# Kernel tuning notes

Hardware: AMD Instinct MI355X
Metric: run time of the kernel (lower is better)

Reference implementation:

```python
import jax, jax.numpy as jnp
import numpy as np

B, N, D, P = 64, 1024, 256, 256


def setup_inputs() -> dict:
    key = jax.random.key(0)
    kx, k1, k2, k4 = jax.random.split(key, 4)
    x = jax.random.normal(kx, (B, N, D), dtype=jnp.float32)
    # weights ~ random_uniform(-0.05, 0.05) in the original; scale here is irrelevant for math
    w1 = jax.random.uniform(k1, (D, P), dtype=jnp.float32, minval=-0.05, maxval=0.05)
    w2 = jax.random.uniform(k2, (D, P), dtype=jnp.float32, minval=-0.05, maxval=0.05)
    w4 = jax.random.uniform(k4, (P, 1), dtype=jnp.float32, minval=-0.05, maxval=0.05)
    return {"x": x, "w1": w1, "w2": w2, "w4": w4}


def reference(x, w1, w2, w4):
    # x: [B, N, D] (already stacked/transposed; query_n=key_n=values=x in the original)
    q = jax.nn.sigmoid(jnp.einsum('bnd,dp->bnp', x, w1))  # [B,N,P]
    k = jax.nn.sigmoid(jnp.einsum('bnd,dp->bnp', x, w2))  # [B,N,P]
    temper = jnp.sqrt(jnp.asarray(w1.shape[1], x.dtype))
    attn = jax.nn.softmax(jnp.einsum('bnp,bmp->bnm', q, k) / temper, axis=2)  # [B,N,N]
    # dropout(0.1) in the original is inference-identity here
    out = jnp.einsum('bnm,bmd->bnd', attn, x)             # [B,N,D]
    a = jax.nn.softmax(jnp.einsum('bnd,do->bno', out, w4), axis=1)  # [B,N,1]
    sentence = jnp.sum(x * a, axis=1)                     # [B,D]
    return sentence
```

## Files before the change

### kernel.cpp

```cpp
#include <hip/hip_runtime.h>
#include <hip/hip_bf16.h>
#include <cstdint>
#include <cstddef>

constexpr int BB = 64;
constexpr int NN = 1024;
constexpr int DD = 256;
constexpr int PP = 256;

typedef short short8 __attribute__((ext_vector_type(8)));
typedef float f32x4 __attribute__((ext_vector_type(4)));

constexpr float LOG2E = 1.4426950408889634f;

__device__ __forceinline__ unsigned short f2bf(float f) {
    union { __hip_bfloat16 h; unsigned short u; } v;
    v.h = __float2bfloat16(f);
    return v.u;
}

__device__ __forceinline__ float fsigmoid(float x) {
    return __builtin_amdgcn_rcpf(1.f + __builtin_amdgcn_exp2f(x * -LOG2E));
}

__device__ __forceinline__ void pin8(short8& v) {
    asm volatile("" : "+v"(v));
}

__device__ __forceinline__ void async_load16(void* lds, const void* g) {
    __builtin_amdgcn_global_load_lds(
        (const __attribute__((address_space(1))) unsigned int*)g,
        (__attribute__((address_space(3))) unsigned int*)lds, 16, 0, 0);
}

__device__ __forceinline__ void stage256(const unsigned short* base,
                                         unsigned short* lds, int wv, int lane) {
    char* dst0 = (char*)lds + wv * 16384;
    #pragma unroll
    for (int i = 0; i < 16; i++) {
        int row = wv * 32 + i * 2 + (lane >> 5);
        int blk = (lane & 31) ^ (row & 7);
        async_load16(dst0 + i * 1024, (const char*)base + row * 512 + blk * 16);
    }
}

__device__ __forceinline__ short8 lds_frag(const unsigned short* lds, int row, int kidx) {
    uint32_t byte = (uint32_t)(row * 512) + (uint32_t)(((kidx ^ (row & 7)) & 31) << 4);
    return *reinterpret_cast<const short8*>(reinterpret_cast<const char*>(lds) + byte);
}

__global__ void prep_wt(const float* __restrict__ w1, const float* __restrict__ w2,
                        unsigned short* __restrict__ wt) {
    int j = blockIdx.x;
    int d = threadIdx.x;
    const float* w = (j < PP) ? w1 : w2;
    int jj = j & (PP - 1);
    wt[j * DD + d] = f2bf(w[d * PP + jj]);
}

__global__ __launch_bounds__(512, 2) void qk_fused(const float* __restrict__ x,
                                                   const unsigned short* __restrict__ wt,
                                                   const float* __restrict__ w4,
                                                   unsigned short* __restrict__ qb,
                                                   unsigned short* __restrict__ kb,
                                                   float* __restrict__ xv) {
    __shared__ __align__(16) unsigned short wl[256 * 256];
    const int t = threadIdx.x, wv = t >> 6, lane = t & 63, l15 = lane & 15, l4 = lane >> 4;
    const int rowBase = blockIdx.x * 256 + wv * 32;

    stage256(wt, wl, wv, lane);

    short8 xf[2][8];
    float xvp[2] = {0.f, 0.f};
    #pragma unroll
    for (int kc = 0; kc < 8; kc++) {
        float4 w4a = *reinterpret_cast<const float4*>(w4 + kc * 32 + l4 * 8);
        float4 w4b = *reinterpret_cast<const float4*>(w4 + kc * 32 + l4 * 8 + 4);
        #pragma unroll
        for (int s = 0; s < 2; s++) {
            const float* xr = x + (size_t)(rowBase + s * 16 + l15) * DD + kc * 32 + l4 * 8;
            float4 a = *reinterpret_cast<const float4*>(xr);
            float4 b = *reinterpret_cast<const float4*>(xr + 4);
            xvp[s] += a.x * w4a.x + a.y * w4a.y + a.z * w4a.z + a.w * w4a.w
                    + b.x * w4b.x + b.y * w4b.y + b.z * w4b.z + b.w * w4b.w;
            short8 f;
            f[0] = (short)f2bf(a.x); f[1] = (short)f2bf(a.y);
            f[2] = (short)f2bf(a.z); f[3] = (short)f2bf(a.w);
            f[4] = (short)f2bf(b.x); f[5] = (short)f2bf(b.y);
            f[6] = (short)f2bf(b.z); f[7] = (short)f2bf(b.w);
            xf[s][kc] = f;
        }
    }
    #pragma unroll
    for (int s = 0; s < 2; s++)
        #pragma unroll
        for (int kc = 0; kc < 8; kc++) pin8(xf[s][kc]);
    #pragma unroll
    for (int s = 0; s < 2; s++) {
        xvp[s] += __shfl_xor(xvp[s], 16);
        xvp[s] += __shfl_xor(xvp[s], 32);
        if (l4 == 0) xv[rowBase + s * 16 + l15] = xvp[s];
    }

    __syncthreads();

    #pragma unroll 1
    for (int h = 0; h < 2; h++) {
        if (h == 1) {
            __syncthreads();
            stage256(wt + 256 * DD, wl, wv, lane);
            __syncthreads();
        }
        unsigned short* outp = h ? kb : qb;
        #pragma unroll 1
        for (int pt = 0; pt < 16; pt++) {
            f32x4 acc0 = {0.f, 0.f, 0.f, 0.f};
            f32x4 acc1 = {0.f, 0.f, 0.f, 0.f};
            __builtin_amdgcn_s_setprio(1);
            #pragma unroll
            for (int kc = 0; kc < 8; kc++) {
                short8 wf = lds_frag(wl, pt * 16 + l15, kc * 4 + l4);
                acc0 = __builtin_amdgcn_mfma_f32_16x16x32_bf16(wf, xf[0][kc], acc0, 0, 0, 0);
                acc1 = __builtin_amdgcn_mfma_f32_16x16x32_bf16(wf, xf[1][kc], acc1, 0, 0, 0);
            }
            __builtin_amdgcn_s_setprio(0);
            const int pc = pt * 16 + l4 * 4;
            ushort4 pk;
            pk.x = f2bf(fsigmoid(acc0[0]));
            pk.y = f2bf(fsigmoid(acc0[1]));
            pk.z = f2bf(fsigmoid(acc0[2]));
            pk.w = f2bf(fsigmoid(acc0[3]));
            *reinterpret_cast<ushort4*>(outp + (size_t)(rowBase + l15) * PP + pc) = pk;
            pk.x = f2bf(fsigmoid(acc1[0]));
            pk.y = f2bf(fsigmoid(acc1[1]));
            pk.z = f2bf(fsigmoid(acc1[2]));
            pk.w = f2bf(fsigmoid(acc1[3]));
            *reinterpret_cast<ushort4*>(outp + (size_t)(rowBase + 16 + l15) * PP + pc) = pk;
        }
    }
}

__global__ __launch_bounds__(512, 2) void attn_logit(const unsigned short* __restrict__ qb,
                                                     const unsigned short* __restrict__ kb,
                                                     const float* __restrict__ xv,
                                                     float* __restrict__ numo,
                                                     float* __restrict__ deno) {
    __shared__ __align__(16) unsigned short kq[256 * 256];
    __shared__ float xvs[256];
    const int t = threadIdx.x, wv = t >> 6, lane = t & 63, l15 = lane & 15, l4 = lane >> 4;
    const int wg = blockIdx.x;
    const int xcd = wg & 7, r_ = wg >> 3;
    const int quarter = r_ & 3;
    const int b = xcd + 8 * (r_ >> 2);
    const unsigned short* kbb = kb + ((size_t)b * NN + quarter * 256) * PP;

    stage256(kbb, kq, wv, lane);
    if (t < 256) xvs[t] = xv[b * NN + quarter * 256 + t];
    __syncthreads();

    #pragma unroll 1
    for (int p = 0; p < 2; p++) {
        short8 qf[4][8];
        const int q0 = b * NN + p * 512 + wv * 64;
        #pragma unroll
        for (int s = 0; s < 4; s++) {
            const unsigned short* qrow = qb + (size_t)(q0 + s * 16 + l15) * PP;
            #pragma unroll
            for (int kc = 0; kc < 8; kc++)
                qf[s][kc] = *reinterpret_cast<const short8*>(qrow + kc * 32 + l4 * 8);
        }
        #pragma unroll
        for (int s = 0; s < 4; s++)
            #pragma unroll
            for (int kc = 0; kc < 8; kc++) pin8(qf[s][kc]);

        float den[4][4], num[4][4];
        #pragma unroll
        for (int s = 0; s < 4; s++)
            #pragma unroll
            for (int r = 0; r < 4; r++) { den[s][r] = 0.f; num[s][r] = 0.f; }

        #pragma unroll 8
        for (int mc = 0; mc < 16; mc++) {
            f32x4 z = {0.f, 0.f, 0.f, 0.f};
            f32x4 a[4] = {z, z, z, z};
            __builtin_amdgcn_s_setprio(1);
            #pragma unroll
            for (int kc = 0; kc < 8; kc++) {
                short8 kf = lds_frag(kq, mc * 16 + l15, kc * 4 + l4);
                a[0] = __builtin_amdgcn_mfma_f32_16x16x32_bf16(qf[0][kc], kf, a[0], 0, 0, 0);
                a[1] = __builtin_amdgcn_mfma_f32_16x16x32_bf16(qf[1][kc], kf, a[1], 0, 0, 0);
                a[2] = __builtin_amdgcn_mfma_f32_16x16x32_bf16(qf[2][kc], kf, a[2], 0, 0, 0);
                a[3] = __builtin_amdgcn_mfma_f32_16x16x32_bf16(qf[3][kc], kf, a[3], 0, 0, 0);
            }
            __builtin_amdgcn_s_setprio(0);
            float xvv = xvs[mc * 16 + l15];
            #pragma unroll
            for (int s = 0; s < 4; s++)
                #pragma unroll
                for (int r = 0; r < 4; r++) {
                    float e = __builtin_amdgcn_exp2f(a[s][r] * (0.0625f * LOG2E));
                    den[s][r] += e;
                    num[s][r] += e * xvv;
                }
        }
        #pragma unroll
        for (int s = 0; s < 4; s++)
            #pragma unroll
            for (int r = 0; r < 4; r++) {
                #pragma unroll
                for (int off = 1; off < 16; off <<= 1) {
                    den[s][r] += __shfl_xor(den[s][r], off);
                    num[s][r] += __shfl_xor(num[s][r], off);
                }
            }
        if (l15 == 0) {
            #pragma unroll
            for (int s = 0; s < 4; s++)
                #pragma unroll
                for (int r = 0; r < 4; r++) {
                    int n = p * 512 + wv * 64 + s * 16 + l4 * 4 + r;
                    size_t o = (size_t)quarter * BB * NN + (size_t)b * NN + n;
                    numo[o] = num[s][r];
                    deno[o] = den[s][r];
                }
        }
    }
}

__global__ __launch_bounds__(256) void sent_partial(const float* __restrict__ x,
                                                    const float* __restrict__ numo,
                                                    const float* __restrict__ deno,
                                                    float* __restrict__ part) {
    __shared__ float al[64];
    __shared__ float redA[4];
    __shared__ float redB[4];
    const int b = blockIdx.x, ch = blockIdx.y;
    const int t = threadIdx.x;
    float l[4];
    #pragma unroll
    for (int i = 0; i < 4; i++) {
        int n = b * NN + t + i * 256;
        float ns = 0.f, ds = 0.f;
        #pragma unroll
        for (int q = 0; q < 4; q++) {
            ns += numo[(size_t)q * BB * NN + n];
            ds += deno[(size_t)q * BB * NN + n];
        }
        l[i] = ns / ds;
    }
    float mx = fmaxf(fmaxf(l[0], l[1]), fmaxf(l[2], l[3]));
    #pragma unroll
    for (int off = 1; off < 64; off <<= 1) mx = fmaxf(mx, __shfl_xor(mx, off));
    if ((t & 63) == 0) redA[t >> 6] = mx;
    __syncthreads();
    mx = fmaxf(fmaxf(redA[0], redA[1]), fmaxf(redA[2], redA[3]));
    float e[4], es = 0.f;
    #pragma unroll
    for (int i = 0; i < 4; i++) { e[i] = __expf(l[i] - mx); es += e[i]; }
    #pragma unroll
    for (int off = 1; off < 64; off <<= 1) es += __shfl_xor(es, off);
    if ((t & 63) == 0) redB[t >> 6] = es;
    __syncthreads();
    float inv = 1.f / (redB[0] + redB[1] + redB[2] + redB[3]);
    int ei = ch >> 2;
    float sel = (ei == 0) ? e[0] : (ei == 1) ? e[1] : (ei == 2) ? e[2] : e[3];
    if ((t >> 6) == (ch & 3)) al[t & 63] = sel * inv;
    __syncthreads();
    float acc = 0.f;
    const float* xb = x + ((size_t)b * NN + ch * 64) * DD + t;
    #pragma unroll 8
    for (int n = 0; n < 64; n++)
        acc += al[n] * xb[(size_t)n * DD];
    part[(b * 16 + ch) * DD + t] = acc;
}

__global__ void sent_final(const float* __restrict__ part, float* __restrict__ out) {
    int b = blockIdx.x, t = threadIdx.x;
    float s = 0.f;
    #pragma unroll
    for (int c = 0; c < 16; c++) s += part[(b * 16 + c) * DD + t];
    out[b * DD + t] = s;
}

extern "C" void kernel_launch(void* const* d_in, const int* in_sizes, int n_in,
                              void* d_out, int out_size, void* d_ws, size_t ws_size,
                              hipStream_t stream) {
    (void)in_sizes; (void)n_in; (void)out_size; (void)ws_size;
    const float* x  = (const float*)d_in[0];
    const float* w1 = (const float*)d_in[1];
    const float* w2 = (const float*)d_in[2];
    const float* w4 = (const float*)d_in[3];
    float* out = (float*)d_out;

    char* ws = (char*)d_ws;
    const size_t MB = 1024 * 1024;
    unsigned short* qb   = (unsigned short*)(ws);
    unsigned short* kb   = (unsigned short*)(ws + 32 * MB);
    unsigned short* wt   = (unsigned short*)(ws + 64 * MB);
    float*          xv   = (float*)(ws + 64 * MB + 256 * 1024);
    float*          num  = (float*)(ws + 64 * MB + 512 * 1024);
    float*          den  = (float*)(ws + 64 * MB + 1536 * 1024);
    float*          part = (float*)(ws);

    prep_wt<<<dim3(2 * PP), dim3(DD), 0, stream>>>(w1, w2, wt);
    qk_fused<<<dim3(BB * NN / 256), dim3(512), 0, stream>>>(x, wt, w4, qb, kb, xv);
    attn_logit<<<dim3(4 * BB), dim3(512), 0, stream>>>(qb, kb, xv, num, den);
    sent_partial<<<dim3(BB, 16), dim3(256), 0, stream>>>(x, num, den, part);
    sent_final<<<dim3(BB), dim3(DD), 0, stream>>>(part, out);
}
```

Before: 94.35 us.

## Compute K projection inside attn_logit directly into LDS instead of via global

Moves the K = sigmoid(x·W2) projection out of qk_fused and into attn_logit. Each block now loads its 256 rows of x, converts them to bf16, and multiplies them against W2, which is staged 32 columns at a time. The result is written straight into the swizzled LDS tile that used to be filled from kb. This removes the 32 MB bf16 K write and read-back through global memory and halves the projection work in qk_fused. The cost is extra x loads and MFMA work, plus eight barrier-separated W2 staging rounds inside the attention kernel, which may reduce its occupancy or overlap.

```diff
diff --git a/kernel.cpp b/kernel.cpp
--- a/kernel.cpp
+++ b/kernel.cpp
@@ -39,6 +39,17 @@
     #pragma unroll
     for (int i = 0; i < 16; i++) {
         int row = wv * 32 + i * 2 + (lane >> 5);
+        int blk = (lane & 31) ^ (row & 7);
+        async_load16(dst0 + i * 1024, (const char*)base + row * 512 + blk * 16);
+    }
+}
+
+__device__ __forceinline__ void stage32_w8(const unsigned short* base,
+                                           unsigned short* lds, int wv, int lane) {
+    char* dst0 = (char*)lds + wv * 2048;
+    #pragma unroll
+    for (int i = 0; i < 2; i++) {
+        int row = wv * 4 + i * 2 + (lane >> 5);
         int blk = (lane & 31) ^ (row & 7);
         async_load16(dst0 + i * 1024, (const char*)base + row * 512 + blk * 16);
     }
@@ -62,7 +73,6 @@
                                                    const unsigned short* __restrict__ wt,
                                                    const float* __restrict__ w4,
                                                    unsigned short* __restrict__ qb,
-                                                   unsigned short* __restrict__ kb,
                                                    float* __restrict__ xv) {
     __shared__ __align__(16) unsigned short wl[256 * 256];
     const int t = threadIdx.x, wv = t >> 6, lane = t & 63, l15 = lane & 15, l4 = lane >> 4;
@@ -105,58 +115,111 @@
     __syncthreads();
 
     #pragma unroll 1
-    for (int h = 0; h < 2; h++) {
-        if (h == 1) {
-            __syncthreads();
-            stage256(wt + 256 * DD, wl, wv, lane);
-            __syncthreads();
-        }
-        unsigned short* outp = h ? kb : qb;
-        #pragma unroll 1
-        for (int pt = 0; pt < 16; pt++) {
-            f32x4 acc0 = {0.f, 0.f, 0.f, 0.f};
-            f32x4 acc1 = {0.f, 0.f, 0.f, 0.f};
-            __builtin_amdgcn_s_setprio(1);
-            #pragma unroll
-            for (int kc = 0; kc < 8; kc++) {
-                short8 wf = lds_frag(wl, pt * 16 + l15, kc * 4 + l4);
-                acc0 = __builtin_amdgcn_mfma_f32_16x16x32_bf16(wf, xf[0][kc], acc0, 0, 0, 0);
-                acc1 = __builtin_amdgcn_mfma_f32_16x16x32_bf16(wf, xf[1][kc], acc1, 0, 0, 0);
-            }
-            __builtin_amdgcn_s_setprio(0);
-            const int pc = pt * 16 + l4 * 4;
-            ushort4 pk;
-            pk.x = f2bf(fsigmoid(acc0[0]));
-            pk.y = f2bf(fsigmoid(acc0[1]));
-            pk.z = f2bf(fsigmoid(acc0[2]));
-            pk.w = f2bf(fsigmoid(acc0[3]));
-            *reinterpret_cast<ushort4*>(outp + (size_t)(rowBase + l15) * PP + pc) = pk;
-            pk.x = f2bf(fsigmoid(acc1[0]));
-            pk.y = f2bf(fsigmoid(acc1[1]));
-            pk.z = f2bf(fsigmoid(acc1[2]));
-            pk.w = f2bf(fsigmoid(acc1[3]));
-            *reinterpret_cast<ushort4*>(outp + (size_t)(rowBase + 16 + l15) * PP + pc) = pk;
-        }
-    }
-}
-
-__global__ __launch_bounds__(512, 2) void attn_logit(const unsigned short* __restrict__ qb,
-                                                     const unsigned short* __restrict__ kb,
+    for (int pt = 0; pt < 16; pt++) {
+        f32x4 acc0 = {0.f, 0.f, 0.f, 0.f};
+        f32x4 acc1 = {0.f, 0.f, 0.f, 0.f};
+        __builtin_amdgcn_s_setprio(1);
+        #pragma unroll
+        for (int kc = 0; kc < 8; kc++) {
+            short8 wf = lds_frag(wl, pt * 16 + l15, kc * 4 + l4);
+            acc0 = __builtin_amdgcn_mfma_f32_16x16x32_bf16(wf, xf[0][kc], acc0, 0, 0, 0);
+            acc1 = __builtin_amdgcn_mfma_f32_16x16x32_bf16(wf, xf[1][kc], acc1, 0, 0, 0);
+        }
+        __builtin_amdgcn_s_setprio(0);
+        const int pc = pt * 16 + l4 * 4;
+        ushort4 pk;
+        pk.x = f2bf(fsigmoid(acc0[0]));
+        pk.y = f2bf(fsigmoid(acc0[1]));
+        pk.z = f2bf(fsigmoid(acc0[2]));
+        pk.w = f2bf(fsigmoid(acc0[3]));
+        *reinterpret_cast<ushort4*>(qb + (size_t)(rowBase + l15) * PP + pc) = pk;
+        pk.x = f2bf(fsigmoid(acc1[0]));
+        pk.y = f2bf(fsigmoid(acc1[1]));
+        pk.z = f2bf(fsigmoid(acc1[2]));
+        pk.w = f2bf(fsigmoid(acc1[3]));
+        *reinterpret_cast<ushort4*>(qb + (size_t)(rowBase + 16 + l15) * PP + pc) = pk;
+    }
+}
+
+__global__ __launch_bounds__(512, 2) void attn_logit(const float* __restrict__ x,
+                                                     const unsigned short* __restrict__ wt,
+                                                     const unsigned short* __restrict__ qb,
                                                      const float* __restrict__ xv,
                                                      float* __restrict__ numo,
                                                      float* __restrict__ deno) {
     __shared__ __align__(16) unsigned short kq[256 * 256];
+    __shared__ __align__(16) unsigned short wld[32 * 256];
     __shared__ float xvs[256];
     const int t = threadIdx.x, wv = t >> 6, lane = t & 63, l15 = lane & 15, l4 = lane >> 4;
     const int wg = blockIdx.x;
     const int xcd = wg & 7, r_ = wg >> 3;
     const int quarter = r_ & 3;
     const int b = xcd + 8 * (r_ >> 2);
-    const unsigned short* kbb = kb + ((size_t)b * NN + quarter * 256) * PP;
-
-    stage256(kbb, kq, wv, lane);
+    const unsigned short* wt2 = wt + 256 * DD;
+
+    stage32_w8(wt2, wld, wv, lane);
+
+    short8 xf[2][8];
+    const float* xq = x + (size_t)(b * NN + quarter * 256 + wv * 32) * DD;
+    #pragma unroll
+    for (int kc = 0; kc < 8; kc++) {
+        #pragma unroll
+        for (int s = 0; s < 2; s++) {
+            const float* xr = xq + (size_t)(s * 16 + l15) * DD + kc * 32 + l4 * 8;
+            float4 a = *reinterpret_cast<const float4*>(xr);
+            float4 bq = *reinterpret_cast<const float4*>(xr + 4);
+            short8 f;
+            f[0] = (short)f2bf(a.x);  f[1] = (short)f2bf(a.y);
+            f[2] = (short)f2bf(a.z);  f[3] = (short)f2bf(a.w);
+            f[4] = (short)f2bf(bq.x); f[5] = (short)f2bf(bq.y);
+            f[6] = (short)f2bf(bq.z); f[7] = (short)f2bf(bq.w);
+            xf[s][kc] = f;
+        }
+    }
+    #pragma unroll
+    for (int s = 0; s < 2; s++)
+        #pragma unroll
+        for (int kc = 0; kc < 8; kc++) pin8(xf[s][kc]);
     if (t < 256) xvs[t] = xv[b * NN + quarter * 256 + t];
-    __syncthreads();
+
+    __syncthreads();
+
+    #pragma unroll 1
+    for (int c = 0; c < 8; c++) {
+        __builtin_amdgcn_s_setprio(1);
+        #pragma unroll
+        for (int pt = 0; pt < 2; pt++) {
+            f32x4 acc0 = {0.f, 0.f, 0.f, 0.f};
+            f32x4 acc1 = {0.f, 0.f, 0.f, 0.f};
+            #pragma unroll
+            for (int kc = 0; kc < 8; kc++) {
+                short8 wf = lds_frag(wld, pt * 16 + l15, kc * 4 + l4);
+                acc0 = __builtin_amdgcn_mfma_f32_16x16x32_bf16(wf, xf[0][kc], acc0, 0, 0, 0);
+                acc1 = __builtin_amdgcn_mfma_f32_16x16x32_bf16(wf, xf[1][kc], acc1, 0, 0, 0);
+            }
+            const int p0 = c * 32 + pt * 16 + l4 * 4;
+            #pragma unroll
+            for (int s = 0; s < 2; s++) {
+                const f32x4& a = s ? acc1 : acc0;
+                ushort4 pk;
+                pk.x = f2bf(fsigmoid(a[0]));
+                pk.y = f2bf(fsigmoid(a[1]));
+                pk.z = f2bf(fsigmoid(a[2]));
+                pk.w = f2bf(fsigmoid(a[3]));
+                int m = wv * 32 + s * 16 + l15;
+                uint32_t byte = (uint32_t)(m * 512)
+                              + (uint32_t)((((p0 >> 3) ^ (m & 7)) & 31) << 4)
+                              + (uint32_t)((p0 & 7) * 2);
+                *reinterpret_cast<ushort4*>(reinterpret_cast<char*>(kq) + byte) = pk;
+            }
+        }
+        __builtin_amdgcn_s_setprio(0);
+        __syncthreads();
+        if (c < 7) {
+            stage32_w8(wt2 + (size_t)(c + 1) * 32 * DD, wld, wv, lane);
+            __syncthreads();
+        }
+    }
 
     #pragma unroll 1
     for (int p = 0; p < 2; p++) {
@@ -296,7 +359,6 @@
     char* ws = (char*)d_ws;
     const size_t MB = 1024 * 1024;
     unsigned short* qb   = (unsigned short*)(ws);
-    unsigned short* kb   = (unsigned short*)(ws + 32 * MB);
     unsigned short* wt   = (unsigned short*)(ws + 64 * MB);
     float*          xv   = (float*)(ws + 64 * MB + 256 * 1024);
     float*          num  = (float*)(ws + 64 * MB + 512 * 1024);
@@ -304,8 +366,8 @@
     float*          part = (float*)(ws);
 
     prep_wt<<<dim3(2 * PP), dim3(DD), 0, stream>>>(w1, w2, wt);
-    qk_fused<<<dim3(BB * NN / 256), dim3(512), 0, stream>>>(x, wt, w4, qb, kb, xv);
-    attn_logit<<<dim3(4 * BB), dim3(512), 0, stream>>>(qb, kb, xv, num, den);
+    qk_fused<<<dim3(BB * NN / 256), dim3(512), 0, stream>>>(x, wt, w4, qb, xv);
+    attn_logit<<<dim3(4 * BB), dim3(512), 0, stream>>>(x, wt, qb, xv, num, den);
     sent_partial<<<dim3(BB, 16), dim3(256), 0, stream>>>(x, num, den, part);
     sent_final<<<dim3(BB), dim3(DD), 0, stream>>>(part, out);
 }
```

Result: slower. 100.3 us (+6.3%).

## Split attention logit work across twice as many 1024-thread blocks

Applied to the files above, without the earlier changes.

Restructures attn_logit so each block handles half the queries for a key quarter, with 16 waves each owning 32 queries, instead of 8 waves looping over two 64-query passes. The aim is more resident waves per CU to hide latency, and lower per-wave register pressure. In exchange, each K tile is staged into LDS twice as often, and each LDS fragment now feeds only two MFMAs instead of four, which raises LDS read traffic.

```diff
diff --git a/kernel.cpp b/kernel.cpp
--- a/kernel.cpp
+++ b/kernel.cpp
@@ -33,12 +33,23 @@
         (__attribute__((address_space(3))) unsigned int*)lds, 16, 0, 0);
 }
 
-__device__ __forceinline__ void stage256(const unsigned short* base,
-                                         unsigned short* lds, int wv, int lane) {
+__device__ __forceinline__ void stage256_w8(const unsigned short* base,
+                                            unsigned short* lds, int wv, int lane) {
     char* dst0 = (char*)lds + wv * 16384;
     #pragma unroll
     for (int i = 0; i < 16; i++) {
         int row = wv * 32 + i * 2 + (lane >> 5);
+        int blk = (lane & 31) ^ (row & 7);
+        async_load16(dst0 + i * 1024, (const char*)base + row * 512 + blk * 16);
+    }
+}
+
+__device__ __forceinline__ void stage256_w16(const unsigned short* base,
+                                             unsigned short* lds, int wv, int lane) {
+    char* dst0 = (char*)lds + wv * 8192;
+    #pragma unroll
+    for (int i = 0; i < 8; i++) {
+        int row = wv * 16 + i * 2 + (lane >> 5);
         int blk = (lane & 31) ^ (row & 7);
         async_load16(dst0 + i * 1024, (const char*)base + row * 512 + blk * 16);
     }
@@ -68,7 +79,7 @@
     const int t = threadIdx.x, wv = t >> 6, lane = t & 63, l15 = lane & 15, l4 = lane >> 4;
     const int rowBase = blockIdx.x * 256 + wv * 32;
 
-    stage256(wt, wl, wv, lane);
+    stage256_w8(wt, wl, wv, lane);
 
     short8 xf[2][8];
     float xvp[2] = {0.f, 0.f};
@@ -108,7 +119,7 @@
     for (int h = 0; h < 2; h++) {
         if (h == 1) {
             __syncthreads();
-            stage256(wt + 256 * DD, wl, wv, lane);
+            stage256_w8(wt + 256 * DD, wl, wv, lane);
             __syncthreads();
         }
         unsigned short* outp = h ? kb : qb;
@@ -140,91 +151,86 @@
     }
 }
 
-__global__ __launch_bounds__(512, 2) void attn_logit(const unsigned short* __restrict__ qb,
-                                                     const unsigned short* __restrict__ kb,
-                                                     const float* __restrict__ xv,
-                                                     float* __restrict__ numo,
-                                                     float* __restrict__ deno) {
+__global__ __launch_bounds__(1024, 4) void attn_logit(const unsigned short* __restrict__ qb,
+                                                      const unsigned short* __restrict__ kb,
+                                                      const float* __restrict__ xv,
+                                                      float* __restrict__ numo,
+                                                      float* __restrict__ deno) {
     __shared__ __align__(16) unsigned short kq[256 * 256];
     __shared__ float xvs[256];
     const int t = threadIdx.x, wv = t >> 6, lane = t & 63, l15 = lane & 15, l4 = lane >> 4;
     const int wg = blockIdx.x;
     const int xcd = wg & 7, r_ = wg >> 3;
-    const int quarter = r_ & 3;
-    const int b = xcd + 8 * (r_ >> 2);
+    const int qhalf = r_ & 1;
+    const int quarter = (r_ >> 1) & 3;
+    const int b = (r_ >> 3) * 8 + xcd;
     const unsigned short* kbb = kb + ((size_t)b * NN + quarter * 256) * PP;
 
-    stage256(kbb, kq, wv, lane);
+    stage256_w16(kbb, kq, wv, lane);
     if (t < 256) xvs[t] = xv[b * NN + quarter * 256 + t];
     __syncthreads();
 
-    #pragma unroll 1
-    for (int p = 0; p < 2; p++) {
-        short8 qf[4][8];
-        const int q0 = b * NN + p * 512 + wv * 64;
-        #pragma unroll
-        for (int s = 0; s < 4; s++) {
-            const unsigned short* qrow = qb + (size_t)(q0 + s * 16 + l15) * PP;
+    short8 qf[2][8];
+    const int q0 = b * NN + qhalf * 512 + wv * 32;
+    #pragma unroll
+    for (int s = 0; s < 2; s++) {
+        const unsigned short* qrow = qb + (size_t)(q0 + s * 16 + l15) * PP;
+        #pragma unroll
+        for (int kc = 0; kc < 8; kc++)
+            qf[s][kc] = *reinterpret_cast<const short8*>(qrow + kc * 32 + l4 * 8);
+    }
+    #pragma unroll
+    for (int s = 0; s < 2; s++)
+        #pragma unroll
+        for (int kc = 0; kc < 8; kc++) pin8(qf[s][kc]);
+
+    float den[2][4], num[2][4];
+    #pragma unroll
+    for (int s = 0; s < 2; s++)
+        #pragma unroll
+        for (int r = 0; r < 4; r++) { den[s][r] = 0.f; num[s][r] = 0.f; }
+
+    #pragma unroll 8
+    for (int mc = 0; mc < 16; mc++) {
+        f32x4 a0 = {0.f, 0.f, 0.f, 0.f};
+        f32x4 a1 = {0.f, 0.f, 0.f, 0.f};
+        __builtin_amdgcn_s_setprio(1);
+        #pragma unroll
+        for (int kc = 0; kc < 8; kc++) {
+            short8 kf = lds_frag(kq, mc * 16 + l15, kc * 4 + l4);
+            a0 = __builtin_amdgcn_mfma_f32_16x16x32_bf16(qf[0][kc], kf, a0, 0, 0, 0);
+            a1 = __builtin_amdgcn_mfma_f32_16x16x32_bf16(qf[1][kc], kf, a1, 0, 0, 0);
+        }
+        __builtin_amdgcn_s_setprio(0);
+        float xvv = xvs[mc * 16 + l15];
+        #pragma unroll
+        for (int r = 0; r < 4; r++) {
+            float e0 = __builtin_amdgcn_exp2f(a0[r] * (0.0625f * LOG2E));
+            den[0][r] += e0; num[0][r] += e0 * xvv;
+            float e1 = __builtin_amdgcn_exp2f(a1[r] * (0.0625f * LOG2E));
+            den[1][r] += e1; num[1][r] += e1 * xvv;
+        }
+    }
+    #pragma unroll
+    for (int s = 0; s < 2; s++)
+        #pragma unroll
+        for (int r = 0; r < 4; r++) {
             #pragma unroll
-            for (int kc = 0; kc < 8; kc++)
-                qf[s][kc] = *reinterpret_cast<const short8*>(qrow + kc * 32 + l4 * 8);
-        }
-        #pragma unroll
-        for (int s = 0; s < 4; s++)
-            #pragma unroll
-            for (int kc = 0; kc < 8; kc++) pin8(qf[s][kc]);
-
-        float den[4][4], num[4][4];
-        #pragma unroll
-        for (int s = 0; s < 4; s++)
-            #pragma unroll
-            for (int r = 0; r < 4; r++) { den[s][r] = 0.f; num[s][r] = 0.f; }
-
-        #pragma unroll 8
-        for (int mc = 0; mc < 16; mc++) {
-            f32x4 z = {0.f, 0.f, 0.f, 0.f};
-            f32x4 a[4] = {z, z, z, z};
-            __builtin_amdgcn_s_setprio(1);
-            #pragma unroll
-            for (int kc = 0; kc < 8; kc++) {
-                short8 kf = lds_frag(kq, mc * 16 + l15, kc * 4 + l4);
-                a[0] = __builtin_amdgcn_mfma_f32_16x16x32_bf16(qf[0][kc], kf, a[0], 0, 0, 0);
-                a[1] = __builtin_amdgcn_mfma_f32_16x16x32_bf16(qf[1][kc], kf, a[1], 0, 0, 0);
-                a[2] = __builtin_amdgcn_mfma_f32_16x16x32_bf16(qf[2][kc], kf, a[2], 0, 0, 0);
-                a[3] = __builtin_amdgcn_mfma_f32_16x16x32_bf16(qf[3][kc], kf, a[3], 0, 0, 0);
+            for (int off = 1; off < 16; off <<= 1) {
+                den[s][r] += __shfl_xor(den[s][r], off);
+                num[s][r] += __shfl_xor(num[s][r], off);
             }
-            __builtin_amdgcn_s_setprio(0);
-            float xvv = xvs[mc * 16 + l15];
-            #pragma unroll
-            for (int s = 0; s < 4; s++)
-                #pragma unroll
-                for (int r = 0; r < 4; r++) {
-                    float e = __builtin_amdgcn_exp2f(a[s][r] * (0.0625f * LOG2E));
-                    den[s][r] += e;
-                    num[s][r] += e * xvv;
-                }
-        }
-        #pragma unroll
-        for (int s = 0; s < 4; s++)
+        }
+    if (l15 == 0) {
+        #pragma unroll
+        for (int s = 0; s < 2; s++)
             #pragma unroll
             for (int r = 0; r < 4; r++) {
-                #pragma unroll
-                for (int off = 1; off < 16; off <<= 1) {
-                    den[s][r] += __shfl_xor(den[s][r], off);
-                    num[s][r] += __shfl_xor(num[s][r], off);
-                }
+                int n = qhalf * 512 + wv * 32 + s * 16 + l4 * 4 + r;
+                size_t o = (size_t)quarter * BB * NN + (size_t)b * NN + n;
+                numo[o] = num[s][r];
+                deno[o] = den[s][r];
             }
-        if (l15 == 0) {
-            #pragma unroll
-            for (int s = 0; s < 4; s++)
-                #pragma unroll
-                for (int r = 0; r < 4; r++) {
-                    int n = p * 512 + wv * 64 + s * 16 + l4 * 4 + r;
-                    size_t o = (size_t)quarter * BB * NN + (size_t)b * NN + n;
-                    numo[o] = num[s][r];
-                    deno[o] = den[s][r];
-                }
-        }
     }
 }
 
@@ -305,7 +311,7 @@
 
     prep_wt<<<dim3(2 * PP), dim3(DD), 0, stream>>>(w1, w2, wt);
     qk_fused<<<dim3(BB * NN / 256), dim3(512), 0, stream>>>(x, wt, w4, qb, kb, xv);
-    attn_logit<<<dim3(4 * BB), dim3(512), 0, stream>>>(qb, kb, xv, num, den);
+    attn_logit<<<dim3(8 * BB), dim3(1024), 0, stream>>>(qb, kb, xv, num, den);
     sent_partial<<<dim3(BB, 16), dim3(256), 0, stream>>>(x, num, den, part);
     sent_final<<<dim3(BB), dim3(DD), 0, stream>>>(part, out);
 }
```

New measurement: 95.75 us. No clear change (+1.5%).
